# Optimization experiments

Hardware: AMD Instinct MI355X
Metric: run time of the kernel (lower is better)

Reference implementation:

```python
import jax, jax.numpy as jnp
import numpy as np

D_MODEL = 2048
N_HEADS = 8
HEAD_DIM = D_MODEL // N_HEADS
SCALING = HEAD_DIM ** -0.5


def setup_inputs() -> dict:
    key = jax.random.key(0)
    ks = jax.random.split(key, 9)
    B, S, D = 2, 2048, D_MODEL
    std = D ** -0.5
    inp = {"x": jax.random.normal(ks[0], (B, S, D), dtype=jnp.float32)}
    names = ["Wq", "Wk", "Wv", "Wo"]
    for i, n in enumerate(names):
        inp[n] = jax.random.normal(ks[1 + i], (D, D), dtype=jnp.float32) * std
        inp["b" + n[1]] = jax.random.normal(ks[5 + i], (D,), dtype=jnp.float32) * 0.01
    return inp


def reference(x, Wq, bq, Wk, bk, Wv, bv, Wo, bo):
    B, S, D = x.shape
    H, hd = N_HEADS, HEAD_DIM

    def proj(W, b):
        # nn.Linear: x @ W.T + b, then split heads -> [B, H, S, hd]
        y = jnp.einsum("bsd,ed->bse", x, W) + b
        return y.reshape(B, S, H, hd).transpose(0, 2, 1, 3)

    q = proj(Wq, bq)
    k = proj(Wk, bk)
    v = proj(Wv, bv)

    # scaled QK^T: [B, H, S, S]
    attn_weights = jnp.einsum("bhqd,bhkd->bhqk", q, k) * SCALING
    causal = jnp.tril(jnp.ones((S, S), dtype=bool))  # [S, S]
    attn_weights = jnp.where(causal[None, None], attn_weights, -jnp.inf)
    attn_probs = jax.nn.softmax(attn_weights, axis=-1)

    out = jnp.einsum("bhqk,bhkd->bhqd", attn_probs, v)  # [B, H, S, hd]
    out = out.transpose(0, 2, 1, 3).reshape(B, S, D)
    out = jnp.einsum("bsd,ed->bse", out, Wo) + bo
    return (out, attn_probs)
```

## Files before the change

kernel.cpp:

```cpp
#include <hip/hip_runtime.h>
#include <cstdint>
#include <cstddef>

typedef _Float16 f16;
typedef __attribute__((ext_vector_type(4))) _Float16 f16x4;
typedef __attribute__((ext_vector_type(8))) _Float16 f16x8;
typedef __attribute__((ext_vector_type(4))) float f32x4;

#define NB 2
#define SEQ 2048
#define DM 2048
#define NH 8
#define HD 256
#define MT (NB * SEQ)

#define QSCALE 0.09016844f
#define CEXP   23.08312065f

__device__ __forceinline__ void gload16(const f16* g, f16* l) {
    __builtin_amdgcn_global_load_lds(
        (const __attribute__((address_space(1))) uint32_t*)(const void*)g,
        (__attribute__((address_space(3))) uint32_t*)(void*)l,
        16, 0, 0);
}

__global__ __launch_bounds__(256) void k_cvt(const float* __restrict__ src,
                                             f16* __restrict__ dst, int n) {
    for (int i = (blockIdx.x * blockDim.x + threadIdx.x) * 4; i < n;
         i += gridDim.x * blockDim.x * 4) {
        f32x4 v = *(const f32x4*)(src + i);
        f16x4 h;
        h[0] = (f16)v[0]; h[1] = (f16)v[1]; h[2] = (f16)v[2]; h[3] = (f16)v[3];
        *(f16x4*)(dst + i) = h;
    }
}

__device__ __forceinline__ void gemm128_core(const f16* __restrict__ A,
                                             const f16* __restrict__ B,
                                             int m0, int n0,
                                             f16* As, f16* Bs,
                                             f32x4 acc[4][4]) {
    const int tid  = threadIdx.x;
    const int wave = tid >> 6, lane = tid & 63;
    const int wr = (wave >> 1) << 6, wc = (wave & 1) << 6;
    const int lr = lane & 15;
    const int lk = (lane >> 4) << 3;

    for (int k0 = 0; k0 < DM; k0 += 32) {
        __syncthreads();
#pragma unroll
        for (int j = 0; j < 2; ++j) {
            int base = (j * 4 + wave) << 9;
            int flat = base + (lane << 3);
            int r = flat >> 5, c = flat & 31;
            gload16(A + (size_t)(m0 + r) * DM + k0 + c, As + base);
            gload16(B + (size_t)(n0 + r) * DM + k0 + c, Bs + base);
        }
        __syncthreads();
        f16x8 af[4], bf[4];
#pragma unroll
        for (int mi = 0; mi < 4; ++mi)
            af[mi] = *(const f16x8*)&As[(wr + mi * 16 + lr) * 32 + lk];
#pragma unroll
        for (int nj = 0; nj < 4; ++nj)
            bf[nj] = *(const f16x8*)&Bs[(wc + nj * 16 + lr) * 32 + lk];
        __builtin_amdgcn_s_setprio(1);
#pragma unroll
        for (int mi = 0; mi < 4; ++mi)
#pragma unroll
            for (int nj = 0; nj < 4; ++nj)
                acc[mi][nj] = __builtin_amdgcn_mfma_f32_16x16x32_f16(
                    af[mi], bf[nj], acc[mi][nj], 0, 0, 0);
        __builtin_amdgcn_s_setprio(0);
    }
}

__global__ __launch_bounds__(256) void k_proj_qkv(
    const f16* __restrict__ xh, const f16* __restrict__ Wq,
    const f16* __restrict__ Wk, const f16* __restrict__ Wv,
    const float* __restrict__ bq, const float* __restrict__ bk,
    const float* __restrict__ bv,
    f16* __restrict__ Qh, f16* __restrict__ Kh, f16* __restrict__ Vth) {
    __shared__ __align__(16) f16 As[128 * 32];
    __shared__ __align__(16) f16 Bs[128 * 32];
    const int mode = blockIdx.z;
    const f16* W = (mode == 0) ? Wq : (mode == 1) ? Wk : Wv;
    const float* bias = (mode == 0) ? bq : (mode == 1) ? bk : bv;

    const int m0 = blockIdx.y * 128, n0 = blockIdx.x * 128;
    f32x4 acc[4][4];
#pragma unroll
    for (int mi = 0; mi < 4; ++mi)
#pragma unroll
        for (int nj = 0; nj < 4; ++nj) acc[mi][nj] = (f32x4){0.f, 0.f, 0.f, 0.f};

    gemm128_core(xh, W, m0, n0, As, Bs, acc);

    const int lane = threadIdx.x & 63, wave = threadIdx.x >> 6;
    const int wr = (wave >> 1) << 6, wc = (wave & 1) << 6;
    const int lr = lane & 15, lg = lane >> 4;
#pragma unroll
    for (int nj = 0; nj < 4; ++nj) {
        int n = n0 + wc + nj * 16 + lr;
        float bb = bias[n];
        int h = n >> 8, d = n & 255;
#pragma unroll
        for (int mi = 0; mi < 4; ++mi) {
#pragma unroll
            for (int i = 0; i < 4; ++i) {
                int m = m0 + wr + mi * 16 + lg * 4 + i;
                int b = m >> 11, s = m & 2047;
                float v = acc[mi][nj][i] + bb;
                size_t bh = (size_t)(b * NH + h);
                if (mode == 0)
                    Qh[((bh * SEQ + s) << 8) + d] = (f16)(v * QSCALE);
                else if (mode == 1)
                    Kh[((bh * SEQ + s) << 8) + d] = (f16)v;
                else
                    Vth[((bh * HD + d) << 11) + s] = (f16)v;
            }
        }
    }
}

__global__ __launch_bounds__(256) void k_proj_o(
    const f16* __restrict__ Oh, const f16* __restrict__ Wo,
    const float* __restrict__ bo, float* __restrict__ out) {
    __shared__ __align__(16) f16 As[128 * 32];
    __shared__ __align__(16) f16 Bs[128 * 32];
    const int m0 = blockIdx.y * 128, n0 = blockIdx.x * 128;
    f32x4 acc[4][4];
#pragma unroll
    for (int mi = 0; mi < 4; ++mi)
#pragma unroll
        for (int nj = 0; nj < 4; ++nj) acc[mi][nj] = (f32x4){0.f, 0.f, 0.f, 0.f};

    gemm128_core(Oh, Wo, m0, n0, As, Bs, acc);

    const int lane = threadIdx.x & 63, wave = threadIdx.x >> 6;
    const int wr = (wave >> 1) << 6, wc = (wave & 1) << 6;
    const int lr = lane & 15, lg = lane >> 4;
#pragma unroll
    for (int nj = 0; nj < 4; ++nj) {
        int n = n0 + wc + nj * 16 + lr;
        float bb = bo[n];
#pragma unroll
        for (int mi = 0; mi < 4; ++mi) {
#pragma unroll
            for (int i = 0; i < 4; ++i) {
                int m = m0 + wr + mi * 16 + lg * 4 + i;
                out[(size_t)m * DM + n] = acc[mi][nj][i] + bb;
            }
        }
    }
}

__device__ __forceinline__ void stageK(const f16* __restrict__ Kb, int kt,
                                       f16* buf, int wave, int lane) {
#pragma unroll
    for (int j = 0; j < 8; ++j) {
        int base = (j * 4 + wave) << 9;
        int flat = base + (lane << 3);
        int r = flat >> 8;
        int c = (flat & 255) ^ ((r & 7) << 3);
        gload16(Kb + (size_t)(kt * 64 + r) * HD + c, buf + base);
    }
}
__device__ __forceinline__ void stageV(const f16* __restrict__ Vb, int kt,
                                       f16* buf, int wave, int lane) {
#pragma unroll
    for (int j = 0; j < 8; ++j) {
        int base = (j * 4 + wave) << 9;
        int flat = base + (lane << 3);
        int rv = flat >> 6;
        int cv = (flat & 63) ^ ((rv & 3) << 3);
        gload16(Vb + ((size_t)rv << 11) + kt * 64 + cv, buf + base);
    }
}

__global__ __launch_bounds__(256, 2) void k_attn(
    const f16* __restrict__ Qh, const f16* __restrict__ Kh,
    const f16* __restrict__ Vth, float* __restrict__ P,
    f16* __restrict__ Oh) {
    __shared__ __align__(16) f16 B0[64 * 256];
    __shared__ __align__(16) f16 B1[64 * 256];
    __shared__ __align__(16) f16 Ps[4][16][72];

    const int bid = blockIdx.x;
    const int xcd = bid & 7;
    const int slot = bid >> 3;
    const int psel = slot >> 5;
    const int s5 = slot & 31;
    const int qb = psel ? s5 : (31 - s5);
    const int bhid = xcd * 2 + psel;
    const int b = bhid >> 3, h = bhid & 7;

    const int q0 = qb * 64;
    const int tid = threadIdx.x, wave = tid >> 6, lane = tid & 63;
    const int lr = lane & 15, lg = lane >> 4;
    const size_t bh = (size_t)bhid;
    const f16* Qb = Qh + (bh << 19);
    const f16* Kb = Kh + (bh << 19);
    const f16* Vb = Vth + (bh << 19);
    float* Pb = P + (bh << 22);

    const int kswz = (lr & 7) << 3;
    const int vswz = (lr & 3) << 3;

    f16x8 aq[8];
    {
        const f16* qrow = Qb + (size_t)(q0 + wave * 16 + lr) * HD + lg * 8;
#pragma unroll
        for (int kk = 0; kk < 8; ++kk) aq[kk] = *(const f16x8*)(qrow + kk * 32);
    }

    const int rowb = q0 + wave * 16 + lg * 4;
    const int nt = qb + 1;

    float psum[4] = {0.f, 0.f, 0.f, 0.f};

    stageK(Kb, 0, B0, wave, lane);
    __syncthreads();
    for (int kt = 0; kt < nt; ++kt) {
        f16* cur = (kt & 1) ? B1 : B0;
        f16* nxt = (kt & 1) ? B0 : B1;
        if (kt + 1 < nt) stageK(Kb, kt + 1, nxt, wave, lane);
        f32x4 s[4];
#pragma unroll
        for (int nj = 0; nj < 4; ++nj) s[nj] = (f32x4){0.f, 0.f, 0.f, 0.f};
        __builtin_amdgcn_s_setprio(1);
#pragma unroll
        for (int kk = 0; kk < 8; ++kk) {
#pragma unroll
            for (int nj = 0; nj < 4; ++nj) {
                f16x8 bk = *(const f16x8*)&cur[(nj * 16 + lr) * 256 +
                                               ((kk * 32 + lg * 8) ^ kswz)];
                s[nj] = __builtin_amdgcn_mfma_f32_16x16x32_f16(aq[kk], bk, s[nj], 0, 0, 0);
            }
        }
        __builtin_amdgcn_s_setprio(0);
        const int colb = kt * 64 + lr;
#pragma unroll
        for (int i = 0; i < 4; ++i) {
            int row = rowb + i;
#pragma unroll
            for (int nj = 0; nj < 4; ++nj)
                psum[i] += (colb + nj * 16 <= row) ? exp2f(s[nj][i] - CEXP) : 0.f;
        }
        __syncthreads();
    }

    float inv[4];
#pragma unroll
    for (int i = 0; i < 4; ++i) {
        float l = psum[i];
        l += __shfl_xor(l, 1);
        l += __shfl_xor(l, 2);
        l += __shfl_xor(l, 4);
        l += __shfl_xor(l, 8);
        inv[i] = 1.f / l;
    }

    f32x4 o[16];
#pragma unroll
    for (int n = 0; n < 16; ++n) o[n] = (f32x4){0.f, 0.f, 0.f, 0.f};

    stageK(Kb, 0, B0, wave, lane);
    for (int kt = 0; kt < nt; ++kt) {
        stageV(Vb, kt, B1, wave, lane);
        asm volatile("s_waitcnt vmcnt(8)" ::: "memory");
        __builtin_amdgcn_s_barrier();
        __builtin_amdgcn_sched_barrier(0);

        f32x4 s[4];
#pragma unroll
        for (int nj = 0; nj < 4; ++nj) s[nj] = (f32x4){0.f, 0.f, 0.f, 0.f};
        __builtin_amdgcn_s_setprio(1);
#pragma unroll
        for (int kk = 0; kk < 8; ++kk) {
#pragma unroll
            for (int nj = 0; nj < 4; ++nj) {
                f16x8 bk = *(const f16x8*)&B0[(nj * 16 + lr) * 256 +
                                              ((kk * 32 + lg * 8) ^ kswz)];
                s[nj] = __builtin_amdgcn_mfma_f32_16x16x32_f16(aq[kk], bk, s[nj], 0, 0, 0);
            }
        }
        __builtin_amdgcn_s_setprio(0);
#pragma unroll
        for (int i = 0; i < 4; ++i) {
            int row = rowb + i;
#pragma unroll
            for (int nj = 0; nj < 4; ++nj) {
                int col = kt * 64 + nj * 16 + lr;
                float pv = (col <= row) ? exp2f(s[nj][i] - CEXP) * inv[i] : 0.f;
                Ps[wave][lg * 4 + i][nj * 16 + lr] = (f16)pv;
            }
        }
        asm volatile("s_waitcnt vmcnt(0)" ::: "memory");
        __builtin_amdgcn_s_barrier();
        __builtin_amdgcn_sched_barrier(0);

        if (kt + 1 < nt) stageK(Kb, kt + 1, B0, wave, lane);

#pragma unroll
        for (int h2 = 0; h2 < 2; ++h2) {
            int rr = h2 * 8 + (lane >> 3);
            int cc = (lane & 7) * 8;
            f16x8 ph = *(const f16x8*)&Ps[wave][rr][cc];
            int row = q0 + wave * 16 + rr;
            float* dst = Pb + (size_t)row * SEQ + kt * 64 + cc;
            f32x4 lo = {(float)ph[0], (float)ph[1], (float)ph[2], (float)ph[3]};
            f32x4 hi = {(float)ph[4], (float)ph[5], (float)ph[6], (float)ph[7]};
            *(f32x4*)dst = lo;
            *(f32x4*)(dst + 4) = hi;
        }

        __builtin_amdgcn_s_setprio(1);
#pragma unroll
        for (int kk2 = 0; kk2 < 2; ++kk2) {
            f16x8 pa = *(const f16x8*)&Ps[wave][lr][kk2 * 32 + lg * 8];
#pragma unroll
            for (int n = 0; n < 16; ++n) {
                f16x8 bv = *(const f16x8*)&B1[(n * 16 + lr) * 64 +
                                              ((kk2 * 32 + lg * 8) ^ vswz)];
                o[n] = __builtin_amdgcn_mfma_f32_16x16x32_f16(pa, bv, o[n], 0, 0, 0);
            }
        }
        __builtin_amdgcn_s_setprio(0);
        asm volatile("" ::: "memory");
        __builtin_amdgcn_s_barrier();
        __builtin_amdgcn_sched_barrier(0);
    }

    int kstart = (qb + 1) * 64;
    if (kstart < SEQ) {
        f32x4 z = (f32x4){0.f, 0.f, 0.f, 0.f};
        for (int r = 0; r < 64; ++r) {
            float* rp = Pb + (size_t)(q0 + r) * SEQ;
            for (int c = kstart + tid * 4; c < SEQ; c += 1024)
                *(f32x4*)(rp + c) = z;
        }
    }

#pragma unroll
    for (int n = 0; n < 16; ++n) {
#pragma unroll
        for (int i = 0; i < 4; ++i) {
            int row = rowb + i;
            int d = n * 16 + lr;
            Oh[((size_t)b * SEQ + row) * DM + h * HD + d] = (f16)o[n][i];
        }
    }
}

extern "C" void kernel_launch(void* const* d_in, const int* in_sizes, int n_in,
                              void* d_out, int out_size, void* d_ws, size_t ws_size,
                              hipStream_t stream) {
    const float* x  = (const float*)d_in[0];
    const float* Wq = (const float*)d_in[1];
    const float* bq = (const float*)d_in[2];
    const float* Wk = (const float*)d_in[3];
    const float* bk = (const float*)d_in[4];
    const float* Wv = (const float*)d_in[5];
    const float* bv = (const float*)d_in[6];
    const float* Wo = (const float*)d_in[7];
    const float* bo = (const float*)d_in[8];

    float* out  = (float*)d_out;
    float* Pout = out + (size_t)MT * DM;

    f16* xh  = (f16*)Pout;
    f16* Wqh = xh + (size_t)MT * DM;
    f16* Wkh = Wqh + (size_t)DM * DM;
    f16* Wvh = Wkh + (size_t)DM * DM;

    f16* ws16 = (f16*)d_ws;
    f16* Woh = ws16;
    f16* Qh  = Woh + (size_t)DM * DM;
    f16* Kh  = Qh + (size_t)8388608;
    f16* Vth = Kh + (size_t)8388608;
    f16* Oh  = Vth + (size_t)8388608;
    if (ws_size < (size_t)(4194304 + 4 * 8388608) * sizeof(f16)) return;

    k_cvt<<<2048, 256, 0, stream>>>(x, xh, MT * DM);
    k_cvt<<<1024, 256, 0, stream>>>(Wq, Wqh, DM * DM);
    k_cvt<<<1024, 256, 0, stream>>>(Wk, Wkh, DM * DM);
    k_cvt<<<1024, 256, 0, stream>>>(Wv, Wvh, DM * DM);
    k_cvt<<<1024, 256, 0, stream>>>(Wo, Woh, DM * DM);

    dim3 g1(DM / 128, MT / 128, 3);
    k_proj_qkv<<<g1, 256, 0, stream>>>(xh, Wqh, Wkh, Wvh, bq, bk, bv, Qh, Kh, Vth);

    k_attn<<<dim3(512), 256, 0, stream>>>(Qh, Kh, Vth, Pout, Oh);

    dim3 g3(DM / 128, MT / 128, 1);
    k_proj_o<<<g3, 256, 0, stream>>>(Oh, Woh, bo, out);
}
```

Baseline: 397.1 us.

## Rewrite projection GEMMs as 256x128 tiles with triple-buffered swizzled LDS pipeline

Replaces the 128x128, two-sync-per-step projection GEMM core with a 256x128 tile run by 512 threads, a K step of 64, and a three-stage LDS ring filled by global_load_lds. Waits use a vmcnt count and one barrier per step, so loads for step k+2 overlap compute on step k. LDS columns are XOR-swizzled to avoid bank conflicts, and fragment reads are interleaved with MFMA groups. The cost is larger LDS use (144 KB) and one block per CU, and the attention kernel, which likely dominates the total time, is not touched.

```diff
diff --git a/kernel.cpp b/kernel.cpp
--- a/kernel.cpp
+++ b/kernel.cpp
@@ -35,80 +35,167 @@
     }
 }
 
-__device__ __forceinline__ void gemm128_core(const f16* __restrict__ A,
-                                             const f16* __restrict__ B,
-                                             int m0, int n0,
-                                             f16* As, f16* Bs,
-                                             f32x4 acc[4][4]) {
-    const int tid  = threadIdx.x;
-    const int wave = tid >> 6, lane = tid & 63;
-    const int wr = (wave >> 1) << 6, wc = (wave & 1) << 6;
-    const int lr = lane & 15;
-    const int lk = (lane >> 4) << 3;
-
-    for (int k0 = 0; k0 < DM; k0 += 32) {
-        __syncthreads();
-#pragma unroll
-        for (int j = 0; j < 2; ++j) {
-            int base = (j * 4 + wave) << 9;
-            int flat = base + (lane << 3);
-            int r = flat >> 5, c = flat & 31;
-            gload16(A + (size_t)(m0 + r) * DM + k0 + c, As + base);
-            gload16(B + (size_t)(n0 + r) * DM + k0 + c, Bs + base);
-        }
-        __syncthreads();
-        f16x8 af[4], bf[4];
-#pragma unroll
-        for (int mi = 0; mi < 4; ++mi)
-            af[mi] = *(const f16x8*)&As[(wr + mi * 16 + lr) * 32 + lk];
-#pragma unroll
-        for (int nj = 0; nj < 4; ++nj)
-            bf[nj] = *(const f16x8*)&Bs[(wc + nj * 16 + lr) * 32 + lk];
-        __builtin_amdgcn_s_setprio(1);
-#pragma unroll
-        for (int mi = 0; mi < 4; ++mi)
-#pragma unroll
-            for (int nj = 0; nj < 4; ++nj)
-                acc[mi][nj] = __builtin_amdgcn_mfma_f32_16x16x32_f16(
-                    af[mi], bf[nj], acc[mi][nj], 0, 0, 0);
-        __builtin_amdgcn_s_setprio(0);
-    }
-}
-
-__global__ __launch_bounds__(256) void k_proj_qkv(
+
+__device__ __forceinline__ void stage6(const f16* __restrict__ A,
+                                       const f16* __restrict__ B,
+                                       int m0, int n0, int k0,
+                                       f16* AL, f16* BL, int tid) {
+#pragma unroll
+    for (int j = 0; j < 4; ++j) {
+        int flat = j * 4096 + tid * 8;
+        int r = flat >> 6, c = flat & 63;
+        int cs = c ^ ((r & 7) << 3);
+        gload16(A + (size_t)(m0 + r) * DM + k0 + cs,
+                AL + j * 4096 + (tid >> 6) * 512);
+    }
+#pragma unroll
+    for (int j = 0; j < 2; ++j) {
+        int flat = j * 4096 + tid * 8;
+        int r = flat >> 6, c = flat & 63;
+        int cs = c ^ ((r & 7) << 3);
+        gload16(B + (size_t)(n0 + r) * DM + k0 + cs,
+                BL + j * 4096 + (tid >> 6) * 512);
+    }
+}
+
+__device__ __forceinline__ f16x8 rdfrag(const f16* buf, int rowbase, int lr,
+                                        int lg, int kk) {
+    int row = rowbase + lr;
+    int c = (kk * 32 + lg * 8) ^ ((lr & 7) << 3);
+    return *(const f16x8*)&buf[row * 64 + c];
+}
+
+__device__ __forceinline__ void gemm256x128_core(const f16* __restrict__ A,
+                                                 const f16* __restrict__ B,
+                                                 int m0, int n0,
+                                                 f16* AL, f16* BL,
+                                                 f32x4 acc[4][4]) {
+    const int tid = threadIdx.x, wave = tid >> 6, lane = tid & 63;
+    const int wm = wave >> 1, wn = wave & 1;
+    const int lr = lane & 15, lg = lane >> 4;
+    const int nt = DM / 64;
+
+    stage6(A, B, m0, n0, 0, AL, BL, tid);
+    stage6(A, B, m0, n0, 64, AL + 16384, BL + 8192, tid);
+
+    for (int kt = 0; kt < nt; ++kt) {
+        if (kt + 1 < nt) asm volatile("s_waitcnt vmcnt(6)" ::: "memory");
+        else             asm volatile("s_waitcnt vmcnt(0)" ::: "memory");
+        __builtin_amdgcn_s_barrier();
+        __builtin_amdgcn_sched_barrier(0);
+
+        const f16* Ab = AL + (kt % 3) * 16384;
+        const f16* Bb = BL + (kt % 3) * 8192;
+        const int arb = wm * 64, brb = wn * 64;
+
+        f16x8 a0[2][2], b0[2][2];
+#pragma unroll
+        for (int mf = 0; mf < 2; ++mf)
+#pragma unroll
+            for (int kk = 0; kk < 2; ++kk)
+                a0[mf][kk] = rdfrag(Ab, arb + mf * 16, lr, lg, kk);
+#pragma unroll
+        for (int nf = 0; nf < 2; ++nf)
+#pragma unroll
+            for (int kk = 0; kk < 2; ++kk)
+                b0[nf][kk] = rdfrag(Bb, brb + nf * 16, lr, lg, kk);
+
+        if (kt + 2 < nt)
+            stage6(A, B, m0, n0, (kt + 2) * 64,
+                   AL + ((kt + 2) % 3) * 16384, BL + ((kt + 2) % 3) * 8192, tid);
+
+        __builtin_amdgcn_s_setprio(1);
+#pragma unroll
+        for (int mi = 0; mi < 2; ++mi)
+#pragma unroll
+            for (int nj = 0; nj < 2; ++nj)
+#pragma unroll
+                for (int kk = 0; kk < 2; ++kk)
+                    acc[mi][nj] = __builtin_amdgcn_mfma_f32_16x16x32_f16(
+                        a0[mi][kk], b0[nj][kk], acc[mi][nj], 0, 0, 0);
+        __builtin_amdgcn_s_setprio(0);
+
+        f16x8 b1[2][2];
+#pragma unroll
+        for (int nf = 0; nf < 2; ++nf)
+#pragma unroll
+            for (int kk = 0; kk < 2; ++kk)
+                b1[nf][kk] = rdfrag(Bb, brb + 32 + nf * 16, lr, lg, kk);
+        __builtin_amdgcn_s_setprio(1);
+#pragma unroll
+        for (int mi = 0; mi < 2; ++mi)
+#pragma unroll
+            for (int nj = 0; nj < 2; ++nj)
+#pragma unroll
+                for (int kk = 0; kk < 2; ++kk)
+                    acc[mi][nj + 2] = __builtin_amdgcn_mfma_f32_16x16x32_f16(
+                        a0[mi][kk], b1[nj][kk], acc[mi][nj + 2], 0, 0, 0);
+        __builtin_amdgcn_s_setprio(0);
+
+        f16x8 a1[2][2];
+#pragma unroll
+        for (int mf = 0; mf < 2; ++mf)
+#pragma unroll
+            for (int kk = 0; kk < 2; ++kk)
+                a1[mf][kk] = rdfrag(Ab, arb + 32 + mf * 16, lr, lg, kk);
+        __builtin_amdgcn_s_setprio(1);
+#pragma unroll
+        for (int mi = 0; mi < 2; ++mi)
+#pragma unroll
+            for (int nj = 0; nj < 2; ++nj)
+#pragma unroll
+                for (int kk = 0; kk < 2; ++kk)
+                    acc[mi + 2][nj] = __builtin_amdgcn_mfma_f32_16x16x32_f16(
+                        a1[mi][kk], b0[nj][kk], acc[mi + 2][nj], 0, 0, 0);
+        __builtin_amdgcn_s_setprio(0);
+
+        __builtin_amdgcn_s_setprio(1);
+#pragma unroll
+        for (int mi = 0; mi < 2; ++mi)
+#pragma unroll
+            for (int nj = 0; nj < 2; ++nj)
+#pragma unroll
+                for (int kk = 0; kk < 2; ++kk)
+                    acc[mi + 2][nj + 2] = __builtin_amdgcn_mfma_f32_16x16x32_f16(
+                        a1[mi][kk], b1[nj][kk], acc[mi + 2][nj + 2], 0, 0, 0);
+        __builtin_amdgcn_s_setprio(0);
+    }
+}
+
+__global__ __launch_bounds__(512, 1) void k_proj_qkv(
     const f16* __restrict__ xh, const f16* __restrict__ Wq,
     const f16* __restrict__ Wk, const f16* __restrict__ Wv,
     const float* __restrict__ bq, const float* __restrict__ bk,
     const float* __restrict__ bv,
     f16* __restrict__ Qh, f16* __restrict__ Kh, f16* __restrict__ Vth) {
-    __shared__ __align__(16) f16 As[128 * 32];
-    __shared__ __align__(16) f16 Bs[128 * 32];
+    __shared__ __align__(16) f16 AL[3 * 16384];
+    __shared__ __align__(16) f16 BL[3 * 8192];
     const int mode = blockIdx.z;
     const f16* W = (mode == 0) ? Wq : (mode == 1) ? Wk : Wv;
     const float* bias = (mode == 0) ? bq : (mode == 1) ? bk : bv;
 
-    const int m0 = blockIdx.y * 128, n0 = blockIdx.x * 128;
+    const int m0 = blockIdx.y * 256, n0 = blockIdx.x * 128;
     f32x4 acc[4][4];
 #pragma unroll
     for (int mi = 0; mi < 4; ++mi)
 #pragma unroll
         for (int nj = 0; nj < 4; ++nj) acc[mi][nj] = (f32x4){0.f, 0.f, 0.f, 0.f};
 
-    gemm128_core(xh, W, m0, n0, As, Bs, acc);
+    gemm256x128_core(xh, W, m0, n0, AL, BL, acc);
 
     const int lane = threadIdx.x & 63, wave = threadIdx.x >> 6;
-    const int wr = (wave >> 1) << 6, wc = (wave & 1) << 6;
+    const int wm = wave >> 1, wn = wave & 1;
     const int lr = lane & 15, lg = lane >> 4;
 #pragma unroll
     for (int nj = 0; nj < 4; ++nj) {
-        int n = n0 + wc + nj * 16 + lr;
+        int n = n0 + wn * 64 + nj * 16 + lr;
         float bb = bias[n];
         int h = n >> 8, d = n & 255;
 #pragma unroll
         for (int mi = 0; mi < 4; ++mi) {
 #pragma unroll
             for (int i = 0; i < 4; ++i) {
-                int m = m0 + wr + mi * 16 + lg * 4 + i;
+                int m = m0 + wm * 64 + mi * 16 + lg * 4 + i;
                 int b = m >> 11, s = m & 2047;
                 float v = acc[mi][nj][i] + bb;
                 size_t bh = (size_t)(b * NH + h);
@@ -123,32 +210,32 @@
     }
 }
 
-__global__ __launch_bounds__(256) void k_proj_o(
+__global__ __launch_bounds__(512, 1) void k_proj_o(
     const f16* __restrict__ Oh, const f16* __restrict__ Wo,
     const float* __restrict__ bo, float* __restrict__ out) {
-    __shared__ __align__(16) f16 As[128 * 32];
-    __shared__ __align__(16) f16 Bs[128 * 32];
-    const int m0 = blockIdx.y * 128, n0 = blockIdx.x * 128;
+    __shared__ __align__(16) f16 AL[3 * 16384];
+    __shared__ __align__(16) f16 BL[3 * 8192];
+    const int m0 = blockIdx.y * 256, n0 = blockIdx.x * 128;
     f32x4 acc[4][4];
 #pragma unroll
     for (int mi = 0; mi < 4; ++mi)
 #pragma unroll
         for (int nj = 0; nj < 4; ++nj) acc[mi][nj] = (f32x4){0.f, 0.f, 0.f, 0.f};
 
-    gemm128_core(Oh, Wo, m0, n0, As, Bs, acc);
+    gemm256x128_core(Oh, Wo, m0, n0, AL, BL, acc);
 
     const int lane = threadIdx.x & 63, wave = threadIdx.x >> 6;
-    const int wr = (wave >> 1) << 6, wc = (wave & 1) << 6;
+    const int wm = wave >> 1, wn = wave & 1;
     const int lr = lane & 15, lg = lane >> 4;
 #pragma unroll
     for (int nj = 0; nj < 4; ++nj) {
-        int n = n0 + wc + nj * 16 + lr;
+        int n = n0 + wn * 64 + nj * 16 + lr;
         float bb = bo[n];
 #pragma unroll
         for (int mi = 0; mi < 4; ++mi) {
 #pragma unroll
             for (int i = 0; i < 4; ++i) {
-                int m = m0 + wr + mi * 16 + lg * 4 + i;
+                int m = m0 + wm * 64 + mi * 16 + lg * 4 + i;
                 out[(size_t)m * DM + n] = acc[mi][nj][i] + bb;
             }
         }
@@ -388,11 +475,11 @@
     k_cvt<<<1024, 256, 0, stream>>>(Wv, Wvh, DM * DM);
     k_cvt<<<1024, 256, 0, stream>>>(Wo, Woh, DM * DM);
 
-    dim3 g1(DM / 128, MT / 128, 3);
-    k_proj_qkv<<<g1, 256, 0, stream>>>(xh, Wqh, Wkh, Wvh, bq, bk, bv, Qh, Kh, Vth);
+    dim3 g1(DM / 128, MT / 256, 3);
+    k_proj_qkv<<<g1, 512, 0, stream>>>(xh, Wqh, Wkh, Wvh, bq, bk, bv, Qh, Kh, Vth);
 
     k_attn<<<dim3(512), 256, 0, stream>>>(Qh, Kh, Vth, Pout, Oh);
 
-    dim3 g3(DM / 128, MT / 128, 1);
-    k_proj_o<<<g3, 256, 0, stream>>>(Oh, Woh, bo, out);
-}
+    dim3 g3(DM / 128, MT / 256, 1);
+    k_proj_o<<<g3, 512, 0, stream>>>(Oh, Woh, bo, out);
+}
```

After: 376.7 us. 1.05x faster.
